# Kernel optimization log

Hardware: AMD Instinct MI355X
Metric: run time of the kernel (lower is better)

## Reference

```python
import jax, jax.numpy as jnp
import numpy as np

B, S, D, H = 4, 1024, 1024, 16
HD = D // H  # 64, even for RoPE


def _rope_tables(seq_len, head_dim):
    inv_freq = 1.0 / (10000.0 ** (jnp.arange(0, head_dim, 2, dtype=jnp.float32) / head_dim))
    pos = jnp.arange(seq_len, dtype=jnp.float32)
    ang = pos[:, None] * inv_freq[None, :]           # [S, HD/2]
    return jnp.cos(ang), jnp.sin(ang)


def _apply_rope(x, cos, sin):
    # x: [B, S, H, HD]; cos/sin: [S, HD/2] broadcast to [1, S, 1, HD/2]
    c = cos[None, :, None, :]
    s = sin[None, :, None, :]
    x1 = x[..., 0::2]
    x2 = x[..., 1::2]
    return jnp.concatenate([x1 * c - x2 * s, x1 * s + x2 * c], axis=-1)


def setup_inputs() -> dict:
    key = jax.random.key(0)
    ks = jax.random.split(key, 11)
    sc = 1.0 / np.sqrt(D)
    inp = {
        "query": jax.random.normal(ks[0], (B, S, D), jnp.float32),
        "key": jax.random.normal(ks[1], (B, S, D), jnp.float32),
        "value": jax.random.normal(ks[2], (B, S, D), jnp.float32),
        "mask": jnp.tril(jnp.ones((S, S), jnp.int32))[None, None],  # causal [1,1,S,S]
        "Wq": jax.random.normal(ks[3], (D, D), jnp.float32) * sc,
        "bq": jnp.zeros((D,), jnp.float32),
        "Wk": jax.random.normal(ks[4], (D, D), jnp.float32) * sc,
        "bk": jnp.zeros((D,), jnp.float32),
        "Wv": jax.random.normal(ks[5], (D, D), jnp.float32) * sc,
        "bv": jnp.zeros((D,), jnp.float32),
        "Wo": jax.random.normal(ks[6], (D, D), jnp.float32) * sc,
        "bo": jnp.zeros((D,), jnp.float32),
    }
    return inp


def reference(query, key, value, mask, Wq, bq, Wk, bk, Wv, bv, Wo, bo):
    Bq, Sq, _ = query.shape
    Sk = key.shape[1]
    q = (query @ Wq + bq).reshape(Bq, Sq, H, HD)
    k = (key @ Wk + bk).reshape(Bq, Sk, H, HD)
    v = (value @ Wv + bv).reshape(Bq, Sk, H, HD)
    cos, sin = _rope_tables(max(Sq, Sk), HD)
    q = _apply_rope(q, cos[:Sq], sin[:Sq])
    k = _apply_rope(k, cos[:Sk], sin[:Sk])
    scores = jnp.einsum("bqhd,bkhd->bhqk", q, k) / jnp.sqrt(jnp.float32(HD))
    scores = jnp.where(mask == 0, jnp.float32(-jnp.inf), scores)
    attn = jax.nn.softmax(scores, axis=-1)  # dropout p=0 (inference)
    ctx = jnp.einsum("bhqk,bkhd->bqhd", attn, v).reshape(Bq, Sq, D)
    return ctx @ Wo + bo
```

## Files before the change

kernel.cpp:

```cpp
#include <hip/hip_runtime.h>
#include <hip/hip_bf16.h>
#include <math.h>

#define B_DIM 4
#define S_DIM 1024
#define D_DIM 1024
#define H_DIM 16
#define HD_DIM 64
#define M_TOT 4096

typedef short short8 __attribute__((ext_vector_type(8)));
typedef float f32x4 __attribute__((ext_vector_type(4)));

__device__ inline float bf2f(short u)
{
    return __uint_as_float(((unsigned)(unsigned short)u) << 16);
}

__device__ inline void gload_lds16(const void* gsrc, void* lds)
{
    __builtin_amdgcn_global_load_lds(
        (const __attribute__((address_space(1))) unsigned int*)gsrc,
        (__attribute__((address_space(3))) unsigned int*)lds, 16, 0, 0);
}

__global__ __launch_bounds__(256) void rope_table_kernel(float* __restrict__ tab)
{
    const int t = blockIdx.x * 256 + threadIdx.x;
    const int pos = t >> 5, i = t & 31;
    float inv = powf(10000.0f, -(float)(2 * i) / 64.0f);
    float ang = (float)pos * inv;
    float s, c;
    sincosf(ang, &s, &c);
    tab[t] = c;
    tab[32768 + t] = s;
}

__global__ __launch_bounds__(256) void transpose4_to_bf16_kernel(
    const float* __restrict__ W0, const float* __restrict__ W1,
    const float* __restrict__ W2, const float* __restrict__ W3,
    __hip_bfloat16* __restrict__ T0, __hip_bfloat16* __restrict__ T1,
    __hip_bfloat16* __restrict__ T2, __hip_bfloat16* __restrict__ T3)
{
    const float* W = (blockIdx.z == 0) ? W0 : (blockIdx.z == 1) ? W1
                    : (blockIdx.z == 2) ? W2 : W3;
    __hip_bfloat16* T = (blockIdx.z == 0) ? T0 : (blockIdx.z == 1) ? T1
                       : (blockIdx.z == 2) ? T2 : T3;

    __shared__ float tile[32][33];
    const int tid = threadIdx.x;
    const int r = tid >> 3;
    const int c4 = (tid & 7) * 4;

    float4 v = *(const float4*)&W[(long)(blockIdx.y * 32 + r) * D_DIM + blockIdx.x * 32 + c4];
    tile[r][c4 + 0] = v.x;
    tile[r][c4 + 1] = v.y;
    tile[r][c4 + 2] = v.z;
    tile[r][c4 + 3] = v.w;
    __syncthreads();

    __hip_bfloat16 o[4];
    o[0] = __float2bfloat16(tile[c4 + 0][r]);
    o[1] = __float2bfloat16(tile[c4 + 1][r]);
    o[2] = __float2bfloat16(tile[c4 + 2][r]);
    o[3] = __float2bfloat16(tile[c4 + 3][r]);
    *(uint2*)&T[(long)(blockIdx.x * 32 + r) * D_DIM + blockIdx.y * 32 + c4] = *(uint2*)o;
}

__global__ __launch_bounds__(256, 3) void gemm_qkv_kernel(
    const float* __restrict__ Xq, const float* __restrict__ Xk,
    const float* __restrict__ Xv,
    const __hip_bfloat16* __restrict__ WtQ, const __hip_bfloat16* __restrict__ WtK,
    const __hip_bfloat16* __restrict__ WtV,
    const float* __restrict__ bq, const float* __restrict__ bk,
    const float* __restrict__ bv,
    __hip_bfloat16* __restrict__ Qo, __hip_bfloat16* __restrict__ Ko,
    __hip_bfloat16* __restrict__ Vto)
{
    __shared__ __align__(16) __hip_bfloat16 Al[128][40];
    __shared__ __align__(16) __hip_bfloat16 Bl[128][32];

    const int F = blockIdx.x + 8 * blockIdx.y + 256 * blockIdx.z;
    const int xcd = F & 7;
    const int s = F >> 3;
    const int z = s >> 5;
    const int n0 = (s & 7) * 128;
    const int m0 = ((xcd << 2) | ((s >> 3) & 3)) * 128;

    const float* X = (z == 0) ? Xq : (z == 1) ? Xk : Xv;
    const __hip_bfloat16* Wt = (z == 0) ? WtQ : (z == 1) ? WtK : WtV;
    const float* bias = (z == 0) ? bq : (z == 1) ? bk : bv;

    const int tid = threadIdx.x;
    const int l = tid & 63;
    const int w = tid >> 6;

    const int srow = w * 16 + (l >> 2);
    const int skc = (l & 3) * 8;
    const __hip_bfloat16* Bbase = Wt + (long)(n0 + srow) * D_DIM + skc;
    char* ldsB0 = (char*)&Bl[0][0] + w * 1024;

    const int arow = tid >> 1;
    const int ak = (tid & 1) * 16;
    const float* Af = X + (long)(m0 + arow) * D_DIM + ak;

    const int lrow = l & 15;
    const int kg = l >> 4;
    const int wr = (w >> 1) * 64;
    const int wc = (w & 1) * 64;

    f32x4 acc[4][4];
#pragma unroll
    for (int i = 0; i < 4; ++i)
#pragma unroll
        for (int j = 0; j < 4; ++j) acc[i][j] = (f32x4){0.f, 0.f, 0.f, 0.f};

    float4 f0 = *(const float4*)(Af);
    float4 f1 = *(const float4*)(Af + 4);
    float4 f2 = *(const float4*)(Af + 8);
    float4 f3 = *(const float4*)(Af + 12);

    for (int k0 = 0; k0 < D_DIM; k0 += 32) {
        float fa[16] = {f0.x, f0.y, f0.z, f0.w, f1.x, f1.y, f1.z, f1.w,
                        f2.x, f2.y, f2.z, f2.w, f3.x, f3.y, f3.z, f3.w};
        __attribute__((aligned(16))) __hip_bfloat16 ab[16];
#pragma unroll
        for (int i = 0; i < 16; ++i) ab[i] = __float2bfloat16(fa[i]);

        __syncthreads();
        *(short8*)&Al[arow][ak]     = ((const short8*)ab)[0];
        *(short8*)&Al[arow][ak + 8] = ((const short8*)ab)[1];
        gload_lds16(Bbase + k0, ldsB0);
        gload_lds16(Bbase + 64 * D_DIM + k0, ldsB0 + 4096);
        __syncthreads();

        if (k0 + 32 < D_DIM) {
            f0 = *(const float4*)(Af + k0 + 32);
            f1 = *(const float4*)(Af + k0 + 36);
            f2 = *(const float4*)(Af + k0 + 40);
            f3 = *(const float4*)(Af + k0 + 44);
        }

        short8 af[4], bf[4];
#pragma unroll
        for (int i = 0; i < 4; ++i)
            af[i] = *(const short8*)&Al[wr + i * 16 + lrow][kg * 8];
#pragma unroll
        for (int j = 0; j < 4; ++j)
            bf[j] = *(const short8*)&Bl[wc + j * 16 + lrow][kg * 8];
#pragma unroll
        for (int i = 0; i < 4; ++i)
#pragma unroll
            for (int j = 0; j < 4; ++j)
                acc[i][j] = __builtin_amdgcn_mfma_f32_16x16x32_bf16(
                    af[i], bf[j], acc[i][j], 0, 0, 0);
    }

#pragma unroll
    for (int i = 0; i < 4; ++i) {
#pragma unroll
        for (int j = 0; j < 4; ++j) {
            const int col = n0 + wc + j * 16 + lrow;
            const float bvs = bias[col];
            const int rbase = m0 + wr + i * 16 + kg * 4;
            if (z < 2) {
                __hip_bfloat16* Out = (z == 0) ? Qo : Ko;
#pragma unroll
                for (int r = 0; r < 4; ++r)
                    Out[(long)(rbase + r) * D_DIM + col] =
                        __float2bfloat16(acc[i][j][r] + bvs);
            } else {
                const int hh = col >> 6, dd = col & 63;
                const int bb = rbase >> 10, s0 = rbase & 1023;
                __hip_bfloat16 o[4];
#pragma unroll
                for (int r = 0; r < 4; ++r)
                    o[r] = __float2bfloat16(acc[i][j][r] + bvs);
                *(uint2*)&Vto[((long)((bb * H_DIM + hh) * HD_DIM + dd)) * S_DIM + s0] =
                    *(uint2*)o;
            }
        }
    }
}

__global__ __launch_bounds__(256, 2) void gemm_wo_kernel(
    const __hip_bfloat16* __restrict__ X, const __hip_bfloat16* __restrict__ Wt,
    const float* __restrict__ bias, float* __restrict__ Out)
{
    __shared__ __align__(16) __hip_bfloat16 Al[128][32];
    __shared__ __align__(16) __hip_bfloat16 Bl[64][32];

    const int F = blockIdx.x;
    const int xcd = F & 7;
    const int s = F >> 3;
    const int n0 = (s & 15) * 64;
    const int m0 = ((xcd << 2) | (s >> 4)) * 128;

    const int tid = threadIdx.x;
    const int l = tid & 63;
    const int w = tid >> 6;

    const int srow = w * 16 + (l >> 2);
    const int skc = (l & 3) * 8;
    const __hip_bfloat16* Abase = X + (long)(m0 + srow) * D_DIM + skc;
    const __hip_bfloat16* Bbase = Wt + (long)(n0 + srow) * D_DIM + skc;
    char* ldsA0 = (char*)&Al[0][0] + w * 1024;
    char* ldsB0 = (char*)&Bl[0][0] + w * 1024;

    const int lrow = l & 15;
    const int kg = l >> 4;
    const int wr = (w >> 1) * 64;
    const int wc = (w & 1) * 32;

    f32x4 acc[4][2];
#pragma unroll
    for (int i = 0; i < 4; ++i)
#pragma unroll
        for (int j = 0; j < 2; ++j) acc[i][j] = (f32x4){0.f, 0.f, 0.f, 0.f};

    for (int k0 = 0; k0 < D_DIM; k0 += 32) {
        __syncthreads();
        gload_lds16(Abase + k0, ldsA0);
        gload_lds16(Abase + 64 * D_DIM + k0, ldsA0 + 4096);
        gload_lds16(Bbase + k0, ldsB0);
        __syncthreads();

        short8 af[4], bf[2];
#pragma unroll
        for (int i = 0; i < 4; ++i)
            af[i] = *(const short8*)&Al[wr + i * 16 + lrow][kg * 8];
#pragma unroll
        for (int j = 0; j < 2; ++j)
            bf[j] = *(const short8*)&Bl[wc + j * 16 + lrow][kg * 8];
#pragma unroll
        for (int i = 0; i < 4; ++i)
#pragma unroll
            for (int j = 0; j < 2; ++j)
                acc[i][j] = __builtin_amdgcn_mfma_f32_16x16x32_bf16(
                    af[i], bf[j], acc[i][j], 0, 0, 0);
    }

#pragma unroll
    for (int i = 0; i < 4; ++i) {
#pragma unroll
        for (int j = 0; j < 2; ++j) {
            const int col = n0 + wc + j * 16 + lrow;
            const float bv = bias[col];
            const int rbase = m0 + wr + i * 16 + kg * 4;
#pragma unroll
            for (int r = 0; r < 4; ++r)
                Out[(long)(rbase + r) * D_DIM + col] = acc[i][j][r] + bv;
        }
    }
}

__global__ __launch_bounds__(256) void rope_bf16_kernel(
    const __hip_bfloat16* __restrict__ Qi, const __hip_bfloat16* __restrict__ Ki,
    __hip_bfloat16* __restrict__ Qo, __hip_bfloat16* __restrict__ Ko,
    const float* __restrict__ tab)
{
    const long t = (long)blockIdx.x * 256 + threadIdx.x;
    const int row = (int)(t >> 7);
    const int slot = (int)(t & 127);
    const int hh = slot >> 3;
    const int p0 = (slot & 7) * 4;
    const int pos = row & (S_DIM - 1);
    const bool isQ = (blockIdx.y == 0);
    const float scale = isQ ? 0.125f : 1.0f;

    const __hip_bfloat16* src = (isQ ? Qi : Ki) + (long)row * D_DIM + hh * HD_DIM;
    __hip_bfloat16* dst = (isQ ? Qo : Ko) + (long)row * D_DIM + hh * HD_DIM;

    short8 xv = *(const short8*)&src[2 * p0];
    float4 cv = *(const float4*)&tab[pos * 32 + p0];
    float4 sv = *(const float4*)&tab[32768 + pos * 32 + p0];
    float cc[4] = {cv.x, cv.y, cv.z, cv.w};
    float ss[4] = {sv.x, sv.y, sv.z, sv.w};

    __hip_bfloat16 o1[4], o2[4];
#pragma unroll
    for (int j = 0; j < 4; ++j) {
        float x1 = bf2f(xv[2 * j]);
        float x2 = bf2f(xv[2 * j + 1]);
        o1[j] = __float2bfloat16((x1 * cc[j] - x2 * ss[j]) * scale);
        o2[j] = __float2bfloat16((x1 * ss[j] + x2 * cc[j]) * scale);
    }
    *(uint2*)&dst[p0]      = *(uint2*)o1;
    *(uint2*)&dst[p0 + 32] = *(uint2*)o2;
}

#define KPAD 72

__global__ __launch_bounds__(256, 2) void attn_mfma_kernel(
    const __hip_bfloat16* __restrict__ Q,
    const __hip_bfloat16* __restrict__ K,
    const __hip_bfloat16* __restrict__ Vt,
    __hip_bfloat16* __restrict__ CTX)
{
    __shared__ __align__(16) __hip_bfloat16 Kl[64][KPAD];
    __shared__ __align__(16) __hip_bfloat16 Vl[64][KPAD];
    __shared__ __align__(16) __hip_bfloat16 Pl[4][32][KPAD];
    __shared__ __align__(16) float aS[4][2][16];

    const int tid = threadIdx.x;
    const int l = tid & 63;
    const int w = tid >> 6;

    const int bid = blockIdx.x + 8 * blockIdx.y + 128 * blockIdx.z;
    const int half = bid >> 8;
    const int idx = bid & 255;
    int qt = idx & 7;
    if (half) qt = 7 - qt;
    const int rest = idx >> 3;
    const int h = rest & 15;
    const int b = (rest >> 4) | (half << 1);

    const int lrow = l & 15;
    const int kg = l >> 4;
    const int kg4 = kg * 4;

    const int q0w = qt * 128 + w * 32;
    const long qrow_base = (long)b * S_DIM + q0w;

    short8 qf[2][2];
#pragma unroll
    for (int m = 0; m < 2; ++m)
#pragma unroll
        for (int ks = 0; ks < 2; ++ks)
            qf[m][ks] = *(const short8*)&Q[(qrow_base + m * 16 + lrow) * D_DIM +
                                           h * HD_DIM + ks * 32 + kg * 8];

    f32x4 ctx[2][4];
#pragma unroll
    for (int m = 0; m < 2; ++m)
#pragma unroll
        for (int d = 0; d < 4; ++d) ctx[m][d] = (f32x4){0.f, 0.f, 0.f, 0.f};
    float mrun[2] = {-1e30f, -1e30f};
    float lrun[2] = {0.f, 0.f};

    const int sr = tid >> 2;
    const int sc2 = (tid & 3) * 16;
    const __hip_bfloat16* Kg = K + ((long)b * S_DIM + sr) * D_DIM + h * HD_DIM + sc2;
    const __hip_bfloat16* Vg = Vt + ((long)((b * H_DIM + h) * HD_DIM) + sr) * S_DIM + sc2;

    const int ktmax = 2 * qt + 1;

    short8 kp0 = *(const short8*)Kg;
    short8 kp1 = *(const short8*)(Kg + 8);
    short8 vp0 = *(const short8*)Vg;
    short8 vp1 = *(const short8*)(Vg + 8);

    for (int kt = 0; kt <= ktmax; ++kt) {
        __syncthreads();
        *(short8*)&Kl[sr][sc2]     = kp0;
        *(short8*)&Kl[sr][sc2 + 8] = kp1;
        *(short8*)&Vl[sr][sc2]     = vp0;
        *(short8*)&Vl[sr][sc2 + 8] = vp1;
        if (kt < ktmax) {
            const __hip_bfloat16* kp = Kg + (long)(kt + 1) * 64 * D_DIM;
            const __hip_bfloat16* vp = Vg + (kt + 1) * 64;
            kp0 = *(const short8*)kp;
            kp1 = *(const short8*)(kp + 8);
            vp0 = *(const short8*)vp;
            vp1 = *(const short8*)(vp + 8);
        }
        __syncthreads();

        if (kt * 64 > q0w + 31) continue;

        f32x4 sac[2][4];
#pragma unroll
        for (int m = 0; m < 2; ++m)
#pragma unroll
            for (int nt = 0; nt < 4; ++nt) sac[m][nt] = (f32x4){0.f, 0.f, 0.f, 0.f};

        short8 kf[4][2];
#pragma unroll
        for (int nt = 0; nt < 4; ++nt)
#pragma unroll
            for (int ks = 0; ks < 2; ++ks)
                kf[nt][ks] = *(const short8*)&Kl[nt * 16 + lrow][ks * 32 + kg * 8];
#pragma unroll
        for (int m = 0; m < 2; ++m)
#pragma unroll
            for (int nt = 0; nt < 4; ++nt)
#pragma unroll
                for (int ks = 0; ks < 2; ++ks)
                    sac[m][nt] = __builtin_amdgcn_mfma_f32_16x16x32_bf16(
                        kf[nt][ks], qf[m][ks], sac[m][nt], 0, 0, 0);

        const bool partial = (kt * 64 + 63 > q0w);
        const int kbase = kt * 64;
#pragma unroll
        for (int m = 0; m < 2; ++m) {
            const int qg = q0w + m * 16 + lrow;
            float s[16];
#pragma unroll
            for (int nt = 0; nt < 4; ++nt)
#pragma unroll
                for (int r = 0; r < 4; ++r) {
                    float v = sac[m][nt][r];
                    if (partial && (kbase + nt * 16 + kg4 + r > qg)) v = -1e30f;
                    s[nt * 4 + r] = v;
                }
            float t8[8];
#pragma unroll
            for (int i = 0; i < 8; ++i) t8[i] = fmaxf(s[i], s[i + 8]);
#pragma unroll
            for (int i = 0; i < 4; ++i) t8[i] = fmaxf(t8[i], t8[i + 4]);
            float mx = fmaxf(fmaxf(t8[0], t8[1]), fmaxf(t8[2], t8[3]));
            mx = fmaxf(mx, __shfl_xor(mx, 16));
            mx = fmaxf(mx, __shfl_xor(mx, 32));
            const float mnew = fmaxf(mrun[m], mx);
            const float alpha = __expf(mrun[m] - mnew);
            mrun[m] = mnew;

            float p0s = 0.f, p1s = 0.f, p2s = 0.f, p3s = 0.f;
            __attribute__((aligned(8))) __hip_bfloat16 pb[16];
#pragma unroll
            for (int i = 0; i < 4; ++i) {
                float p = __expf(s[i] - mnew);      p0s += p; pb[i] = __float2bfloat16(p);
            }
#pragma unroll
            for (int i = 4; i < 8; ++i) {
                float p = __expf(s[i] - mnew);      p1s += p; pb[i] = __float2bfloat16(p);
            }
#pragma unroll
            for (int i = 8; i < 12; ++i) {
                float p = __expf(s[i] - mnew);      p2s += p; pb[i] = __float2bfloat16(p);
            }
#pragma unroll
            for (int i = 12; i < 16; ++i) {
                float p = __expf(s[i] - mnew);      p3s += p; pb[i] = __float2bfloat16(p);
            }
            float sum = (p0s + p1s) + (p2s + p3s);
            sum += __shfl_xor(sum, 16);
            sum += __shfl_xor(sum, 32);
            lrun[m] = lrun[m] * alpha + sum;

            if (kg == 0) aS[w][m][lrow] = alpha;
#pragma unroll
            for (int nt = 0; nt < 4; ++nt)
                *(uint2*)&Pl[w][m * 16 + lrow][nt * 16 + kg4] = *(uint2*)&pb[nt * 4];
        }

#pragma unroll
        for (int m = 0; m < 2; ++m) {
            f32x4 al4 = *(const f32x4*)&aS[w][m][kg4];
#pragma unroll
            for (int dt = 0; dt < 4; ++dt)
#pragma unroll
                for (int r = 0; r < 4; ++r) ctx[m][dt][r] *= al4[r];
        }

        short8 vf[4][2];
#pragma unroll
        for (int dt = 0; dt < 4; ++dt)
#pragma unroll
            for (int ks = 0; ks < 2; ++ks)
                vf[dt][ks] = *(const short8*)&Vl[dt * 16 + lrow][ks * 32 + kg * 8];
#pragma unroll
        for (int m = 0; m < 2; ++m) {
            short8 pf[2];
#pragma unroll
            for (int ks = 0; ks < 2; ++ks)
                pf[ks] = *(const short8*)&Pl[w][m * 16 + lrow][ks * 32 + kg * 8];
#pragma unroll
            for (int dt = 0; dt < 4; ++dt)
#pragma unroll
                for (int ks = 0; ks < 2; ++ks)
                    ctx[m][dt] = __builtin_amdgcn_mfma_f32_16x16x32_bf16(
                        pf[ks], vf[dt][ks], ctx[m][dt], 0, 0, 0);
        }
    }

    if (kg == 0) {
        aS[w][0][lrow] = lrun[0];
        aS[w][1][lrow] = lrun[1];
    }
#pragma unroll
    for (int m = 0; m < 2; ++m) {
        f32x4 lv = *(const f32x4*)&aS[w][m][kg4];
#pragma unroll
        for (int r = 0; r < 4; ++r) {
            const float inv_l = 1.0f / lv[r];
            const long rowoff = (qrow_base + m * 16 + kg4 + r) * D_DIM + h * HD_DIM;
#pragma unroll
            for (int dt = 0; dt < 4; ++dt)
                CTX[rowoff + dt * 16 + lrow] = __float2bfloat16(ctx[m][dt][r] * inv_l);
        }
    }
}

extern "C" void kernel_launch(void* const* d_in, const int* in_sizes, int n_in,
                              void* d_out, int out_size, void* d_ws, size_t ws_size,
                              hipStream_t stream)
{
    const float* query = (const float*)d_in[0];
    const float* key   = (const float*)d_in[1];
    const float* value = (const float*)d_in[2];
    const float* Wq = (const float*)d_in[4];
    const float* bq = (const float*)d_in[5];
    const float* Wk = (const float*)d_in[6];
    const float* bk = (const float*)d_in[7];
    const float* Wv = (const float*)d_in[8];
    const float* bv = (const float*)d_in[9];
    const float* Wo = (const float*)d_in[10];
    const float* bo = (const float*)d_in[11];

    char* wsb = (char*)d_ws;
    __hip_bfloat16* Qw    = (__hip_bfloat16*)(wsb);
    __hip_bfloat16* Kw    = (__hip_bfloat16*)(wsb + (8L  << 20));
    __hip_bfloat16* Vtb   = (__hip_bfloat16*)(wsb + (16L << 20));
    __hip_bfloat16* Qbf   = (__hip_bfloat16*)(wsb + (24L << 20));
    __hip_bfloat16* Kbf   = (__hip_bfloat16*)(wsb + (32L << 20));
    __hip_bfloat16* CTXbf = (__hip_bfloat16*)(wsb + (40L << 20));
    __hip_bfloat16* WtQ   = (__hip_bfloat16*)(wsb + (48L << 20));
    __hip_bfloat16* WtK   = (__hip_bfloat16*)(wsb + (50L << 20));
    __hip_bfloat16* WtV   = (__hip_bfloat16*)(wsb + (52L << 20));
    __hip_bfloat16* WtO   = (__hip_bfloat16*)(wsb + (54L << 20));
    float*          tab   = (float*)(wsb + (56L << 20));

    rope_table_kernel<<<128, 256, 0, stream>>>(tab);
    transpose4_to_bf16_kernel<<<dim3(32, 32, 4), 256, 0, stream>>>(
        Wq, Wk, Wv, Wo, WtQ, WtK, WtV, WtO);

    gemm_qkv_kernel<<<dim3(8, 32, 3), 256, 0, stream>>>(
        query, key, value, WtQ, WtK, WtV, bq, bk, bv, Qw, Kw, Vtb);

    rope_bf16_kernel<<<dim3(2048, 2), 256, 0, stream>>>(Qw, Kw, Qbf, Kbf, tab);

    attn_mfma_kernel<<<dim3(8, 16, 4), 256, 0, stream>>>(Qbf, Kbf, Vtb, CTXbf);

    gemm_wo_kernel<<<512, 256, 0, stream>>>(CTXbf, WtO, bo, (float*)d_out);
}
```

Baseline: 116.5 us.

## Fuse RoPE into QKV GEMM epilogue and pre-convert activations to bf16

Removes the standalone RoPE kernel by applying rotary embedding and the Q scale inside the QKV GEMM epilogue, pairing even and odd columns with a lane shuffle. Adds a separate kernel that converts query, key and value to bf16 up front, so the GEMM can load A tiles straight into LDS with direct global-to-LDS loads instead of converting fp32 in registers. This saves one full read and write of Q and K, but adds an extra pass over the three fp32 inputs and scattered per-element epilogue stores with table lookups.

```diff
diff --git a/kernel.cpp b/kernel.cpp
--- a/kernel.cpp
+++ b/kernel.cpp
@@ -36,6 +36,24 @@
     tab[32768 + t] = s;
 }
 
+__global__ __launch_bounds__(256) void convert3_kernel(
+    const float* __restrict__ S0, const float* __restrict__ S1,
+    const float* __restrict__ S2,
+    __hip_bfloat16* __restrict__ D0, __hip_bfloat16* __restrict__ D1,
+    __hip_bfloat16* __restrict__ D2)
+{
+    const float* src = (blockIdx.y == 0) ? S0 : (blockIdx.y == 1) ? S1 : S2;
+    __hip_bfloat16* dst = (blockIdx.y == 0) ? D0 : (blockIdx.y == 1) ? D1 : D2;
+    const int base = (blockIdx.x * 256 + threadIdx.x) * 4;
+    float4 v = *(const float4*)(src + base);
+    __hip_bfloat16 o[4];
+    o[0] = __float2bfloat16(v.x);
+    o[1] = __float2bfloat16(v.y);
+    o[2] = __float2bfloat16(v.z);
+    o[3] = __float2bfloat16(v.w);
+    *(uint2*)(dst + base) = *(uint2*)o;
+}
+
 __global__ __launch_bounds__(256) void transpose4_to_bf16_kernel(
     const float* __restrict__ W0, const float* __restrict__ W1,
     const float* __restrict__ W2, const float* __restrict__ W3,
@@ -68,16 +86,17 @@
 }
 
 __global__ __launch_bounds__(256, 3) void gemm_qkv_kernel(
-    const float* __restrict__ Xq, const float* __restrict__ Xk,
-    const float* __restrict__ Xv,
+    const __hip_bfloat16* __restrict__ Xq, const __hip_bfloat16* __restrict__ Xk,
+    const __hip_bfloat16* __restrict__ Xv,
     const __hip_bfloat16* __restrict__ WtQ, const __hip_bfloat16* __restrict__ WtK,
     const __hip_bfloat16* __restrict__ WtV,
     const float* __restrict__ bq, const float* __restrict__ bk,
     const float* __restrict__ bv,
     __hip_bfloat16* __restrict__ Qo, __hip_bfloat16* __restrict__ Ko,
-    __hip_bfloat16* __restrict__ Vto)
-{
-    __shared__ __align__(16) __hip_bfloat16 Al[128][40];
+    __hip_bfloat16* __restrict__ Vto,
+    const float* __restrict__ tab)
+{
+    __shared__ __align__(16) __hip_bfloat16 Al[128][32];
     __shared__ __align__(16) __hip_bfloat16 Bl[128][32];
 
     const int F = blockIdx.x + 8 * blockIdx.y + 256 * blockIdx.z;
@@ -87,114 +106,9 @@
     const int n0 = (s & 7) * 128;
     const int m0 = ((xcd << 2) | ((s >> 3) & 3)) * 128;
 
-    const float* X = (z == 0) ? Xq : (z == 1) ? Xk : Xv;
+    const __hip_bfloat16* X = (z == 0) ? Xq : (z == 1) ? Xk : Xv;
     const __hip_bfloat16* Wt = (z == 0) ? WtQ : (z == 1) ? WtK : WtV;
     const float* bias = (z == 0) ? bq : (z == 1) ? bk : bv;
-
-    const int tid = threadIdx.x;
-    const int l = tid & 63;
-    const int w = tid >> 6;
-
-    const int srow = w * 16 + (l >> 2);
-    const int skc = (l & 3) * 8;
-    const __hip_bfloat16* Bbase = Wt + (long)(n0 + srow) * D_DIM + skc;
-    char* ldsB0 = (char*)&Bl[0][0] + w * 1024;
-
-    const int arow = tid >> 1;
-    const int ak = (tid & 1) * 16;
-    const float* Af = X + (long)(m0 + arow) * D_DIM + ak;
-
-    const int lrow = l & 15;
-    const int kg = l >> 4;
-    const int wr = (w >> 1) * 64;
-    const int wc = (w & 1) * 64;
-
-    f32x4 acc[4][4];
-#pragma unroll
-    for (int i = 0; i < 4; ++i)
-#pragma unroll
-        for (int j = 0; j < 4; ++j) acc[i][j] = (f32x4){0.f, 0.f, 0.f, 0.f};
-
-    float4 f0 = *(const float4*)(Af);
-    float4 f1 = *(const float4*)(Af + 4);
-    float4 f2 = *(const float4*)(Af + 8);
-    float4 f3 = *(const float4*)(Af + 12);
-
-    for (int k0 = 0; k0 < D_DIM; k0 += 32) {
-        float fa[16] = {f0.x, f0.y, f0.z, f0.w, f1.x, f1.y, f1.z, f1.w,
-                        f2.x, f2.y, f2.z, f2.w, f3.x, f3.y, f3.z, f3.w};
-        __attribute__((aligned(16))) __hip_bfloat16 ab[16];
-#pragma unroll
-        for (int i = 0; i < 16; ++i) ab[i] = __float2bfloat16(fa[i]);
-
-        __syncthreads();
-        *(short8*)&Al[arow][ak]     = ((const short8*)ab)[0];
-        *(short8*)&Al[arow][ak + 8] = ((const short8*)ab)[1];
-        gload_lds16(Bbase + k0, ldsB0);
-        gload_lds16(Bbase + 64 * D_DIM + k0, ldsB0 + 4096);
-        __syncthreads();
-
-        if (k0 + 32 < D_DIM) {
-            f0 = *(const float4*)(Af + k0 + 32);
-            f1 = *(const float4*)(Af + k0 + 36);
-            f2 = *(const float4*)(Af + k0 + 40);
-            f3 = *(const float4*)(Af + k0 + 44);
-        }
-
-        short8 af[4], bf[4];
-#pragma unroll
-        for (int i = 0; i < 4; ++i)
-            af[i] = *(const short8*)&Al[wr + i * 16 + lrow][kg * 8];
-#pragma unroll
-        for (int j = 0; j < 4; ++j)
-            bf[j] = *(const short8*)&Bl[wc + j * 16 + lrow][kg * 8];
-#pragma unroll
-        for (int i = 0; i < 4; ++i)
-#pragma unroll
-            for (int j = 0; j < 4; ++j)
-                acc[i][j] = __builtin_amdgcn_mfma_f32_16x16x32_bf16(
-                    af[i], bf[j], acc[i][j], 0, 0, 0);
-    }
-
-#pragma unroll
-    for (int i = 0; i < 4; ++i) {
-#pragma unroll
-        for (int j = 0; j < 4; ++j) {
-            const int col = n0 + wc + j * 16 + lrow;
-            const float bvs = bias[col];
-            const int rbase = m0 + wr + i * 16 + kg * 4;
-            if (z < 2) {
-                __hip_bfloat16* Out = (z == 0) ? Qo : Ko;
-#pragma unroll
-                for (int r = 0; r < 4; ++r)
-                    Out[(long)(rbase + r) * D_DIM + col] =
-                        __float2bfloat16(acc[i][j][r] + bvs);
-            } else {
-                const int hh = col >> 6, dd = col & 63;
-                const int bb = rbase >> 10, s0 = rbase & 1023;
-                __hip_bfloat16 o[4];
-#pragma unroll
-                for (int r = 0; r < 4; ++r)
-                    o[r] = __float2bfloat16(acc[i][j][r] + bvs);
-                *(uint2*)&Vto[((long)((bb * H_DIM + hh) * HD_DIM + dd)) * S_DIM + s0] =
-                    *(uint2*)o;
-            }
-        }
-    }
-}
-
-__global__ __launch_bounds__(256, 2) void gemm_wo_kernel(
-    const __hip_bfloat16* __restrict__ X, const __hip_bfloat16* __restrict__ Wt,
-    const float* __restrict__ bias, float* __restrict__ Out)
-{
-    __shared__ __align__(16) __hip_bfloat16 Al[128][32];
-    __shared__ __align__(16) __hip_bfloat16 Bl[64][32];
-
-    const int F = blockIdx.x;
-    const int xcd = F & 7;
-    const int s = F >> 3;
-    const int n0 = (s & 15) * 64;
-    const int m0 = ((xcd << 2) | (s >> 4)) * 128;
 
     const int tid = threadIdx.x;
     const int l = tid & 63;
@@ -210,6 +124,113 @@
     const int lrow = l & 15;
     const int kg = l >> 4;
     const int wr = (w >> 1) * 64;
+    const int wc = (w & 1) * 64;
+
+    f32x4 acc[4][4];
+#pragma unroll
+    for (int i = 0; i < 4; ++i)
+#pragma unroll
+        for (int j = 0; j < 4; ++j) acc[i][j] = (f32x4){0.f, 0.f, 0.f, 0.f};
+
+    for (int k0 = 0; k0 < D_DIM; k0 += 32) {
+        __syncthreads();
+        gload_lds16(Abase + k0, ldsA0);
+        gload_lds16(Abase + 64 * D_DIM + k0, ldsA0 + 4096);
+        gload_lds16(Bbase + k0, ldsB0);
+        gload_lds16(Bbase + 64 * D_DIM + k0, ldsB0 + 4096);
+        __syncthreads();
+
+        short8 af[4], bf[4];
+#pragma unroll
+        for (int i = 0; i < 4; ++i)
+            af[i] = *(const short8*)&Al[wr + i * 16 + lrow][kg * 8];
+#pragma unroll
+        for (int j = 0; j < 4; ++j)
+            bf[j] = *(const short8*)&Bl[wc + j * 16 + lrow][kg * 8];
+#pragma unroll
+        for (int i = 0; i < 4; ++i)
+#pragma unroll
+            for (int j = 0; j < 4; ++j)
+                acc[i][j] = __builtin_amdgcn_mfma_f32_16x16x32_bf16(
+                    af[i], bf[j], acc[i][j], 0, 0, 0);
+    }
+
+    if (z < 2) {
+        __hip_bfloat16* Out = (z == 0) ? Qo : Ko;
+        const float scale = (z == 0) ? 0.125f : 1.0f;
+#pragma unroll
+        for (int i = 0; i < 4; ++i) {
+#pragma unroll
+            for (int j = 0; j < 4; ++j) {
+                const int col = n0 + wc + j * 16 + lrow;
+                const float bvs = bias[col];
+                const int odd = col & 1;
+                const int ip = (col & 63) >> 1;
+                const int ocol = (col & ~63) + ip + (odd ? 32 : 0);
+                const int rbase = m0 + wr + i * 16 + kg * 4;
+#pragma unroll
+                for (int r = 0; r < 4; ++r) {
+                    const int row = rbase + r;
+                    const int pos = row & (S_DIM - 1);
+                    float x = acc[i][j][r] + bvs;
+                    float xo = __shfl_xor(x, 1);
+                    float x1 = odd ? xo : x;
+                    float x2 = odd ? x : xo;
+                    float cv = tab[pos * 32 + ip];
+                    float sv = tab[32768 + pos * 32 + ip];
+                    float res = odd ? (x1 * sv + x2 * cv) : (x1 * cv - x2 * sv);
+                    Out[(long)row * D_DIM + ocol] = __float2bfloat16(res * scale);
+                }
+            }
+        }
+    } else {
+#pragma unroll
+        for (int i = 0; i < 4; ++i) {
+#pragma unroll
+            for (int j = 0; j < 4; ++j) {
+                const int col = n0 + wc + j * 16 + lrow;
+                const float bvs = bias[col];
+                const int hh = col >> 6, dd = col & 63;
+                const int rbase = m0 + wr + i * 16 + kg * 4;
+                const int bb = rbase >> 10, s0 = rbase & 1023;
+                __hip_bfloat16 o[4];
+#pragma unroll
+                for (int r = 0; r < 4; ++r)
+                    o[r] = __float2bfloat16(acc[i][j][r] + bvs);
+                *(uint2*)&Vto[((long)((bb * H_DIM + hh) * HD_DIM + dd)) * S_DIM + s0] =
+                    *(uint2*)o;
+            }
+        }
+    }
+}
+
+__global__ __launch_bounds__(256, 2) void gemm_wo_kernel(
+    const __hip_bfloat16* __restrict__ X, const __hip_bfloat16* __restrict__ Wt,
+    const float* __restrict__ bias, float* __restrict__ Out)
+{
+    __shared__ __align__(16) __hip_bfloat16 Al[128][32];
+    __shared__ __align__(16) __hip_bfloat16 Bl[64][32];
+
+    const int F = blockIdx.x;
+    const int xcd = F & 7;
+    const int s = F >> 3;
+    const int n0 = (s & 15) * 64;
+    const int m0 = ((xcd << 2) | (s >> 4)) * 128;
+
+    const int tid = threadIdx.x;
+    const int l = tid & 63;
+    const int w = tid >> 6;
+
+    const int srow = w * 16 + (l >> 2);
+    const int skc = (l & 3) * 8;
+    const __hip_bfloat16* Abase = X + (long)(m0 + srow) * D_DIM + skc;
+    const __hip_bfloat16* Bbase = Wt + (long)(n0 + srow) * D_DIM + skc;
+    char* ldsA0 = (char*)&Al[0][0] + w * 1024;
+    char* ldsB0 = (char*)&Bl[0][0] + w * 1024;
+
+    const int lrow = l & 15;
+    const int kg = l >> 4;
+    const int wr = (w >> 1) * 64;
     const int wc = (w & 1) * 32;
 
     f32x4 acc[4][2];
@@ -252,41 +273,6 @@
                 Out[(long)(rbase + r) * D_DIM + col] = acc[i][j][r] + bv;
         }
     }
-}
-
-__global__ __launch_bounds__(256) void rope_bf16_kernel(
-    const __hip_bfloat16* __restrict__ Qi, const __hip_bfloat16* __restrict__ Ki,
-    __hip_bfloat16* __restrict__ Qo, __hip_bfloat16* __restrict__ Ko,
-    const float* __restrict__ tab)
-{
-    const long t = (long)blockIdx.x * 256 + threadIdx.x;
-    const int row = (int)(t >> 7);
-    const int slot = (int)(t & 127);
-    const int hh = slot >> 3;
-    const int p0 = (slot & 7) * 4;
-    const int pos = row & (S_DIM - 1);
-    const bool isQ = (blockIdx.y == 0);
-    const float scale = isQ ? 0.125f : 1.0f;
-
-    const __hip_bfloat16* src = (isQ ? Qi : Ki) + (long)row * D_DIM + hh * HD_DIM;
-    __hip_bfloat16* dst = (isQ ? Qo : Ko) + (long)row * D_DIM + hh * HD_DIM;
-
-    short8 xv = *(const short8*)&src[2 * p0];
-    float4 cv = *(const float4*)&tab[pos * 32 + p0];
-    float4 sv = *(const float4*)&tab[32768 + pos * 32 + p0];
-    float cc[4] = {cv.x, cv.y, cv.z, cv.w};
-    float ss[4] = {sv.x, sv.y, sv.z, sv.w};
-
-    __hip_bfloat16 o1[4], o2[4];
-#pragma unroll
-    for (int j = 0; j < 4; ++j) {
-        float x1 = bf2f(xv[2 * j]);
-        float x2 = bf2f(xv[2 * j + 1]);
-        o1[j] = __float2bfloat16((x1 * cc[j] - x2 * ss[j]) * scale);
-        o2[j] = __float2bfloat16((x1 * ss[j] + x2 * cc[j]) * scale);
-    }
-    *(uint2*)&dst[p0]      = *(uint2*)o1;
-    *(uint2*)&dst[p0 + 32] = *(uint2*)o2;
 }
 
 #define KPAD 72
@@ -509,28 +495,29 @@
     const float* bo = (const float*)d_in[11];
 
     char* wsb = (char*)d_ws;
-    __hip_bfloat16* Qw    = (__hip_bfloat16*)(wsb);
-    __hip_bfloat16* Kw    = (__hip_bfloat16*)(wsb + (8L  << 20));
-    __hip_bfloat16* Vtb   = (__hip_bfloat16*)(wsb + (16L << 20));
-    __hip_bfloat16* Qbf   = (__hip_bfloat16*)(wsb + (24L << 20));
-    __hip_bfloat16* Kbf   = (__hip_bfloat16*)(wsb + (32L << 20));
-    __hip_bfloat16* CTXbf = (__hip_bfloat16*)(wsb + (40L << 20));
-    __hip_bfloat16* WtQ   = (__hip_bfloat16*)(wsb + (48L << 20));
-    __hip_bfloat16* WtK   = (__hip_bfloat16*)(wsb + (50L << 20));
-    __hip_bfloat16* WtV   = (__hip_bfloat16*)(wsb + (52L << 20));
-    __hip_bfloat16* WtO   = (__hip_bfloat16*)(wsb + (54L << 20));
-    float*          tab   = (float*)(wsb + (56L << 20));
+    __hip_bfloat16* Xqb   = (__hip_bfloat16*)(wsb);
+    __hip_bfloat16* Xkb   = (__hip_bfloat16*)(wsb + (8L  << 20));
+    __hip_bfloat16* Xvb   = (__hip_bfloat16*)(wsb + (16L << 20));
+    __hip_bfloat16* Qr    = (__hip_bfloat16*)(wsb + (24L << 20));
+    __hip_bfloat16* Kr    = (__hip_bfloat16*)(wsb + (32L << 20));
+    __hip_bfloat16* Vtb   = (__hip_bfloat16*)(wsb + (40L << 20));
+    __hip_bfloat16* CTXbf = (__hip_bfloat16*)(wsb + (48L << 20));
+    __hip_bfloat16* WtQ   = (__hip_bfloat16*)(wsb + (56L << 20));
+    __hip_bfloat16* WtK   = (__hip_bfloat16*)(wsb + (58L << 20));
+    __hip_bfloat16* WtV   = (__hip_bfloat16*)(wsb + (60L << 20));
+    __hip_bfloat16* WtO   = (__hip_bfloat16*)(wsb + (62L << 20));
+    float*          tab   = (float*)(wsb + (64L << 20));
 
     rope_table_kernel<<<128, 256, 0, stream>>>(tab);
     transpose4_to_bf16_kernel<<<dim3(32, 32, 4), 256, 0, stream>>>(
         Wq, Wk, Wv, Wo, WtQ, WtK, WtV, WtO);
+    convert3_kernel<<<dim3(4096, 3), 256, 0, stream>>>(
+        query, key, value, Xqb, Xkb, Xvb);
 
     gemm_qkv_kernel<<<dim3(8, 32, 3), 256, 0, stream>>>(
-        query, key, value, WtQ, WtK, WtV, bq, bk, bv, Qw, Kw, Vtb);
-
-    rope_bf16_kernel<<<dim3(2048, 2), 256, 0, stream>>>(Qw, Kw, Qbf, Kbf, tab);
-
-    attn_mfma_kernel<<<dim3(8, 16, 4), 256, 0, stream>>>(Qbf, Kbf, Vtb, CTXbf);
+        Xqb, Xkb, Xvb, WtQ, WtK, WtV, bq, bk, bv, Qr, Kr, Vtb, tab);
+
+    attn_mfma_kernel<<<dim3(8, 16, 4), 256, 0, stream>>>(Qr, Kr, Vtb, CTXbf);
 
     gemm_wo_kernel<<<512, 256, 0, stream>>>(CTXbf, WtO, bo, (float*)d_out);
 }
```

New measurement: 126.3 us. +8.4%, slower.
